# Kernel tuning notes

Hardware: AMD Instinct MI355X
Metric: run time of the kernel (lower is better)

## Reference

```python
import jax, jax.numpy as jnp
import numpy as np

HEADS = 2


def _log_cpb(h, w, w1, b1, w2):
    # Swin-v2 style continuous relative position bias on an h*w grid.
    yy, xx = jnp.meshgrid(jnp.arange(h), jnp.arange(w), indexing='ij')
    coords = jnp.stack([yy.reshape(-1), xx.reshape(-1)], axis=-1).astype(jnp.float32)  # (L, 2)
    rel = coords[:, None, :] - coords[None, :, :]                                      # (L, L, 2)
    denom = jnp.array([max(h - 1, 1), max(w - 1, 1)], dtype=jnp.float32)
    rel = rel / denom * 8.0
    rel = jnp.sign(rel) * jnp.log2(1.0 + jnp.abs(rel)) / np.float32(np.log2(8.0))
    bias = jax.nn.relu(rel @ w1.T + b1) @ w2.T                                         # (L, L, heads)
    return jnp.transpose(bias, (2, 0, 1))                                              # (heads, L, L)


def setup_inputs() -> dict:
    key = jax.random.key(0)
    ks = jax.random.split(key, 11)
    b, s, c, h, w = 2, 32, 128, 24, 24
    hid, out_ch = 256, 128
    sc = lambda n: 1.0 / np.sqrt(n)
    return {
        'x':      jax.random.normal(ks[0], (b, s, c, h, w), jnp.float32),
        'qk_w':   jax.random.normal(ks[1], (2 * c, c), jnp.float32) * sc(c),
        'v_w':    jax.random.normal(ks[2], (hid, c), jnp.float32) * sc(c),
        'cpb_w1': jax.random.normal(ks[3], (c, 2), jnp.float32) * sc(2),
        'cpb_b1': jax.random.normal(ks[4], (c,), jnp.float32) * 0.02,
        'cpb_w2': jax.random.normal(ks[5], (HEADS, c), jnp.float32) * sc(c),
        'sa_bias': jax.random.uniform(ks[6], (hid, 1, 1), jnp.float32, -sc(c), sc(c)),
        'mlp_w1': jax.random.normal(ks[7], (hid, hid), jnp.float32) * sc(hid),
        'mlp_b1': jax.random.normal(ks[8], (hid,), jnp.float32) * 0.02,
        'mlp_w2': jax.random.normal(ks[9], (out_ch, hid), jnp.float32) * sc(hid),
        'mlp_b2': jax.random.normal(ks[10], (out_ch,), jnp.float32) * 0.02,
    }


def reference(x, qk_w, v_w, cpb_w1, cpb_b1, cpb_w2, sa_bias, mlp_w1, mlp_b1, mlp_w2, mlp_b2):
    b, s, c, h, w = x.shape
    L = h * w
    qkd = c // HEADS
    vd = v_w.shape[0] // HEADS
    xr = x.reshape(b * s, c, L)                                        # flatten (b s) and (h w)
    # QKV via 1x1 convs == channel matmuls
    qk = jnp.einsum('oc,bcl->bol', qk_w, xr)                           # (bs, 2c, L)
    qk = qk.reshape(b * s, 2, HEADS, qkd, L).transpose(1, 0, 2, 4, 3)  # (2, bs, heads, L, d)
    q, k = qk[0], qk[1]
    v = jnp.einsum('oc,bcl->bol', v_w, xr).reshape(b * s, HEADS, vd, L).transpose(0, 1, 3, 2)
    # learned continuous relative position bias, added as SDPA attn_mask
    bias = _log_cpb(h, w, cpb_w1, cpb_b1, cpb_w2)                      # (heads, L, L)
    scale = np.float32(1.0 / np.sqrt(qkd))
    scores = jnp.einsum('bhld,bhmd->bhlm', q, k) * scale + bias[None]
    attn = jax.nn.softmax(scores, axis=-1)
    out = jnp.einsum('bhlm,bhmd->bhld', attn, v)                       # (bs, heads, L, vd)
    out = out.transpose(0, 1, 3, 2).reshape(b, s, HEADS * vd, h, w)
    out = out + sa_bias[None, None]                                    # (b, s, hid, h, w)
    # 1x1-conv MLP with exact GELU
    y = jnp.einsum('oi,bsihw->bsohw', mlp_w1, out) + mlp_b1[None, None, :, None, None]
    y = jax.nn.gelu(y, approximate=False)
    y = jnp.einsum('oi,bsihw->bsohw', mlp_w2, y) + mlp_b2[None, None, :, None, None]
    return y
```

## Files before the change

kernel.cpp:

```cpp
#include <hip/hip_runtime.h>
#include <cstdint>
#include <cstddef>

constexpr int BS   = 64;
constexpr int Cc   = 128;
constexpr int Lc   = 576;
constexpr int VD   = 128;
constexpr int HID  = 256;
constexpr int OUTC = 128;
constexpr int NPIX = BS * Lc;

typedef __bf16 bf16x8 __attribute__((ext_vector_type(8)));
typedef float  f32x4  __attribute__((ext_vector_type(4)));
typedef unsigned short u16x8 __attribute__((ext_vector_type(8)));
typedef unsigned int   u32x4 __attribute__((ext_vector_type(4)));

__device__ __forceinline__ unsigned short f2bf(float f) {
  unsigned int u = __builtin_bit_cast(unsigned int, f);
  u += 0x7fffu + ((u >> 16) & 1u);
  return (unsigned short)(u >> 16);
}
__device__ __forceinline__ float bf2f(unsigned short h) {
  unsigned int u = ((unsigned int)h) << 16;
  return __builtin_bit_cast(float, u);
}
__device__ __forceinline__ unsigned int packhl(float v) {
  unsigned short hi = f2bf(v);
  unsigned short lo = f2bf(v - bf2f(hi));
  return ((unsigned int)hi << 16) | (unsigned int)lo;
}
__device__ __forceinline__ void unpack8(u32x4 a, u32x4 b, bf16x8& hi, bf16x8& lo) {
  u32x4 h, l;
  h[0] = (a[1] & 0xffff0000u) | (a[0] >> 16);
  l[0] = (a[1] << 16)         | (a[0] & 0xffffu);
  h[1] = (a[3] & 0xffff0000u) | (a[2] >> 16);
  l[1] = (a[3] << 16)         | (a[2] & 0xffffu);
  h[2] = (b[1] & 0xffff0000u) | (b[0] >> 16);
  l[2] = (b[1] << 16)         | (b[0] & 0xffffu);
  h[3] = (b[3] & 0xffff0000u) | (b[2] >> 16);
  l[3] = (b[3] << 16)         | (b[2] & 0xffffu);
  hi = __builtin_bit_cast(bf16x8, h);
  lo = __builtin_bit_cast(bf16x8, l);
}

#define MFMA16(a, b, c) __builtin_amdgcn_mfma_f32_16x16x32_bf16((a), (b), (c), 0, 0, 0)

__global__ __launch_bounds__(256) void cpb_kernel(const float* __restrict__ w1,
                                                  const float* __restrict__ b1,
                                                  const float* __restrict__ w2,
                                                  float* __restrict__ tab) {
  int idx = blockIdx.x * 256 + threadIdx.x;
  if (idx >= 47 * 47) return;
  int dy = idx / 47 - 23, dx = idx % 47 - 23;
  float fy = (float)dy * (8.0f / 23.0f);
  float fx = (float)dx * (8.0f / 23.0f);
  fy = copysignf(log2f(1.0f + fabsf(fy)) * (1.0f / 3.0f), fy);
  fx = copysignf(log2f(1.0f + fabsf(fx)) * (1.0f / 3.0f), fx);
  float a0 = 0.f, a1 = 0.f;
  for (int hh = 0; hh < 128; hh++) {
    float hv = fmaxf(w1[2 * hh] * fy + w1[2 * hh + 1] * fx + b1[hh], 0.f);
    a0 += w2[hh] * hv;
    a1 += w2[128 + hh] * hv;
  }
  tab[idx] = a0;
  tab[2209 + idx] = a1;
}

__global__ __launch_bounds__(256) void bias_mat(const float* __restrict__ tab,
                                                unsigned short* __restrict__ biasC) {
  int id = blockIdx.x * 256 + threadIdx.x;
  if (id >= 737280) return;
  int id2 = id % 2560;
  int grp = id / 2560;
  int wave = grp & 3;
  int mt = (grp >> 2) % 36;
  int hh = grp / 144;
  int g = id2 / 512;
  int lane = (id2 >> 3) & 63;
  int k = id2 & 7;
  int e = g * 8 + k;
  unsigned short val = 0;
  if (e < 36) {
    int ln = e >> 2, r = e & 3;
    int nt = wave * 9 + ln;
    int i = mt * 16 + (lane >> 4) * 4 + r;
    int j = nt * 16 + (lane & 15);
    int yi = i / 24, xi = i - yi * 24;
    int yj = j / 24, xj = j - yj * 24;
    val = f2bf(tab[hh * 2209 + (yi - yj + 23) * 47 + (xi - xj + 23)]);
  }
  biasC[id] = val;
}

__global__ __launch_bounds__(256) void prep_w(
    const float* __restrict__ w1, const float* __restrict__ w2,
    const float* __restrict__ qkw, const float* __restrict__ vw,
    unsigned short* __restrict__ w1h, unsigned short* __restrict__ w1l,
    unsigned short* __restrict__ w2h, unsigned short* __restrict__ w2l,
    unsigned short* __restrict__ wqkh, unsigned short* __restrict__ wqkl,
    unsigned short* __restrict__ wvh, unsigned short* __restrict__ wvl) {
  int id = blockIdx.x * 256 + threadIdx.x;
  const float* src;
  unsigned short *dh, *dl;
  int off;
  if (id < 65536)       { src = w1;  dh = w1h;  dl = w1l;  off = id; }
  else if (id < 98304)  { src = w2;  dh = w2h;  dl = w2l;  off = id - 65536; }
  else if (id < 131072) { src = qkw; dh = wqkh; dl = wqkl; off = id - 98304; }
  else if (id < 163840) { src = vw;  dh = wvh;  dl = wvl;  off = id - 131072; }
  else return;
  float v = src[off];
  unsigned short hi = f2bf(v);
  dh[off] = hi;
  dl[off] = f2bf(v - bf2f(hi));
}

__global__ __launch_bounds__(256) void prep_x(const float* __restrict__ x,
                                              unsigned short* __restrict__ xph,
                                              unsigned short* __restrict__ xpl) {
  __shared__ float xt[128 * 65];
  const int l0 = blockIdx.x * 64, bs = blockIdx.y;
  const int t = threadIdx.x;
  const float* xb = x + (size_t)bs * Cc * Lc;
#pragma unroll
  for (int pass = 0; pass < 8; pass++) {
    int f = pass * 1024 + t * 4;
    int c = f >> 6, ll = f & 63;
    *(float4*)(xt + c * 65 + ll) = *(const float4*)(xb + c * Lc + l0 + ll);
  }
  __syncthreads();
  const int rowl = t >> 2, c0 = (t & 3) * 32;
  const size_t p = (size_t)bs * Lc + l0 + rowl;
  unsigned short hbuf[32], lbuf[32];
#pragma unroll
  for (int i = 0; i < 32; i++) {
    float v = xt[(c0 + i) * 65 + rowl];
    unsigned short hi = f2bf(v);
    hbuf[i] = hi;
    lbuf[i] = f2bf(v - bf2f(hi));
  }
#pragma unroll
  for (int g = 0; g < 4; g++) {
    *(u16x8*)(xph + p * 128 + c0 + g * 8) = *(u16x8*)(hbuf + g * 8);
    *(u16x8*)(xpl + p * 128 + c0 + g * 8) = *(u16x8*)(lbuf + g * 8);
  }
}

__global__ __launch_bounds__(256, 2) void qkv_mfma(
    const unsigned short* __restrict__ xh, const unsigned short* __restrict__ xl,
    const unsigned short* __restrict__ wqkh, const unsigned short* __restrict__ wqkl,
    const unsigned short* __restrict__ wvh, const unsigned short* __restrict__ wvl,
    unsigned short* __restrict__ qg, unsigned short* __restrict__ kg,
    unsigned short* __restrict__ vg) {
  __shared__ unsigned short vt[128 * 130];
  const int t = threadIdx.x;
  const int wv = t >> 6, lane = t & 63;
  const int quad = lane >> 4, cc = lane & 15;
  const int by = blockIdx.y;
  const int m0 = blockIdx.x * 128 + (wv & 1) * 64;
  const int n0 = (wv >> 1) * 64;
  const unsigned short* Wh = (by < 2) ? wqkh : wvh;
  const unsigned short* Wl = (by < 2) ? wqkl : wvl;
  const int wrow0 = (by & 1) * 128 + n0;
  f32x4 acc[4][4];
#pragma unroll
  for (int i = 0; i < 4; i++)
#pragma unroll
    for (int j = 0; j < 4; j++) acc[i][j] = (f32x4){0.f, 0.f, 0.f, 0.f};
  for (int kc = 0; kc < 4; kc++) {
    const int kb = kc * 32 + quad * 8;
    bf16x8 Ah[4], Al[4], Bh[4], Bl[4];
#pragma unroll
    for (int i = 0; i < 4; i++) {
      size_t ar = (size_t)(m0 + i * 16 + cc) * 128 + kb;
      Ah[i] = *(const bf16x8*)(xh + ar);
      Al[i] = *(const bf16x8*)(xl + ar);
      size_t br = (size_t)(wrow0 + i * 16 + cc) * 128 + kb;
      Bh[i] = *(const bf16x8*)(Wh + br);
      Bl[i] = *(const bf16x8*)(Wl + br);
    }
#pragma unroll
    for (int i = 0; i < 4; i++)
#pragma unroll
      for (int j = 0; j < 4; j++) {
        acc[i][j] = MFMA16(Ah[i], Bh[j], acc[i][j]);
        acc[i][j] = MFMA16(Al[i], Bh[j], acc[i][j]);
        acc[i][j] = MFMA16(Ah[i], Bl[j], acc[i][j]);
      }
  }
  if (by < 2) {
    const float sc = (by == 0) ? 0.125f : 1.0f;
#pragma unroll
    for (int j = 0; j < 4; j++) {
      int o = n0 + j * 16 + cc;
#pragma unroll
      for (int i = 0; i < 4; i++)
#pragma unroll
        for (int r = 0; r < 4; r++) {
          int pl = (wv & 1) * 64 + i * 16 + quad * 4 + r;
          vt[pl * 130 + o] = f2bf(acc[i][j][r] * sc);
        }
    }
    __syncthreads();
    unsigned short* dst = (by == 0) ? qg : kg;
    const int pl = t >> 1, head = t & 1;
    const int p = blockIdx.x * 128 + pl;
    const int bs = p / 576, l = p - bs * 576;
    unsigned short* drow = dst + ((size_t)(bs * 2 + head) * Lc + l) * 64;
#pragma unroll
    for (int g = 0; g < 8; g++)
      *(u16x8*)(drow + g * 8) = *(const u16x8*)(vt + pl * 130 + head * 64 + g * 8);
  } else {
    const int head = by - 2;
#pragma unroll
    for (int j = 0; j < 4; j++) {
      int d = n0 + j * 16 + cc;
#pragma unroll
      for (int i = 0; i < 4; i++)
#pragma unroll
        for (int r = 0; r < 4; r++) {
          int pl = (wv & 1) * 64 + i * 16 + quad * 4 + r;
          vt[d * 130 + pl] = f2bf(acc[i][j][r]);
        }
    }
    __syncthreads();
    const int d = t >> 1, half = (t & 1) * 64;
#pragma unroll
    for (int c8 = 0; c8 < 8; c8++) {
      int pl = half + c8 * 8;
      int p = blockIdx.x * 128 + pl;
      int bs = p / 576, l = p - bs * 576;
      *(u16x8*)(vg + ((size_t)(bs * 2 + head) * VD + d) * Lc + l) =
          *(u16x8*)(vt + d * 130 + pl);
    }
  }
}

__global__ __launch_bounds__(256, 4) void attn_kernel(
    const unsigned short* __restrict__ qg,
    const unsigned short* __restrict__ kg,
    const unsigned short* __restrict__ vg,
    const unsigned short* __restrict__ biasC,
    const float* __restrict__ sa_bias,
    unsigned int* __restrict__ aout_p) {
  constexpr int PP = 580;
  __shared__ unsigned short Pb[32 * PP];
  __shared__ float psum[4][32];
  const int pair = blockIdx.x;
  const int hh = pair & 1, bs = pair >> 1;
  const int bm = blockIdx.y;
  const int m0 = bm * 32;
  const int t = threadIdx.x;
  const int wv = t >> 6, lane = t & 63;
  const int quad = lane >> 4, c = lane & 15;
  const unsigned short* qb = qg + ((size_t)pair * Lc + m0) * 64;
  const unsigned short* kb = kg + (size_t)pair * Lc * 64;
  const unsigned short* vb = vg + (size_t)pair * VD * Lc;
  bf16x8 qa0[2], qa1[2];
#pragma unroll
  for (int mt = 0; mt < 2; mt++) {
    const unsigned short* qp = qb + (size_t)(mt * 16 + c) * 64 + quad * 8;
    qa0[mt] = *(const bf16x8*)qp;
    qa1[mt] = *(const bf16x8*)(qp + 32);
  }
  f32x4 S[2][9];
#pragma unroll
  for (int mt = 0; mt < 2; mt++) {
    const unsigned short* bbase =
        biasC + ((((size_t)hh * 36 + (bm * 2 + mt)) * 4 + wv) * 5) * 512;
#pragma unroll
    for (int g = 0; g < 5; g++) {
      u16x8 bv = *(const u16x8*)(bbase + g * 512 + lane * 8);
#pragma unroll
      for (int k = 0; k < 8; k++) {
        int e = g * 8 + k;
        if (e < 36) S[mt][e >> 2][e & 3] = bf2f(bv[k]);
      }
    }
  }
#pragma unroll
  for (int ln = 0; ln < 9; ln++) {
    int nt = wv * 9 + ln;
    const unsigned short* kp = kb + (size_t)(nt * 16 + c) * 64 + quad * 8;
    bf16x8 b0 = *(const bf16x8*)kp;
    bf16x8 b1 = *(const bf16x8*)(kp + 32);
#pragma unroll
    for (int mt = 0; mt < 2; mt++)
      S[mt][ln] = MFMA16(qa1[mt], b1, MFMA16(qa0[mt], b0, S[mt][ln]));
  }
  float sm[2][4] = {{0.f, 0.f, 0.f, 0.f}, {0.f, 0.f, 0.f, 0.f}};
#pragma unroll
  for (int mt = 0; mt < 2; mt++)
#pragma unroll
    for (int ln = 0; ln < 9; ln++)
#pragma unroll
      for (int r = 0; r < 4; r++) {
        float e = __expf(S[mt][ln][r]);
        sm[mt][r] += e;
        Pb[(mt * 16 + quad * 4 + r) * PP + (wv * 9 + ln) * 16 + c] = f2bf(e);
      }
#pragma unroll
  for (int sh = 1; sh < 16; sh <<= 1)
#pragma unroll
    for (int mt = 0; mt < 2; mt++)
#pragma unroll
      for (int r = 0; r < 4; r++) sm[mt][r] += __shfl_xor(sm[mt][r], sh);
  if (c == 0)
#pragma unroll
    for (int mt = 0; mt < 2; mt++)
#pragma unroll
      for (int r = 0; r < 4; r++)
        psum[wv][mt * 16 + quad * 4 + r] = sm[mt][r];
  __syncthreads();
  float inv[2][4];
#pragma unroll
  for (int mt = 0; mt < 2; mt++)
#pragma unroll
    for (int r = 0; r < 4; r++) {
      int row = mt * 16 + quad * 4 + r;
      inv[mt][r] =
          1.0f / (psum[0][row] + psum[1][row] + psum[2][row] + psum[3][row]);
    }
  const int nd0 = wv * 2;
  f32x4 O[2][2];
#pragma unroll
  for (int mt = 0; mt < 2; mt++)
#pragma unroll
    for (int dd = 0; dd < 2; dd++) O[mt][dd] = (f32x4){0.f, 0.f, 0.f, 0.f};
#pragma unroll
  for (int kc = 0; kc < 18; kc++) {
    bf16x8 pa[2];
#pragma unroll
    for (int mt = 0; mt < 2; mt++)
      pa[mt] = *(const bf16x8*)(Pb + (size_t)(mt * 16 + c) * PP + kc * 32 +
                                quad * 8);
#pragma unroll
    for (int dd = 0; dd < 2; dd++) {
      bf16x8 vf = *(const bf16x8*)(vb + (size_t)((nd0 + dd) * 16 + c) * Lc +
                                   kc * 32 + quad * 8);
#pragma unroll
      for (int mt = 0; mt < 2; mt++) O[mt][dd] = MFMA16(pa[mt], vf, O[mt][dd]);
    }
  }
  unsigned int* obp = aout_p + ((size_t)bs * Lc + m0) * HID + hh * 128;
#pragma unroll
  for (int dd = 0; dd < 2; dd++) {
    float sb = sa_bias[hh * 128 + (nd0 + dd) * 16 + c];
#pragma unroll
    for (int mt = 0; mt < 2; mt++)
#pragma unroll
      for (int r = 0; r < 4; r++) {
        float v = O[mt][dd][r] * inv[mt][r] + sb;
        obp[(size_t)(mt * 16 + quad * 4 + r) * HID + (nd0 + dd) * 16 + c] =
            packhl(v);
      }
  }
}

__global__ __launch_bounds__(256, 4) void mlp_fused(
    const unsigned int* __restrict__ ap,
    const unsigned short* __restrict__ w1h, const unsigned short* __restrict__ w1l,
    const float* __restrict__ b1,
    const unsigned short* __restrict__ w2h, const unsigned short* __restrict__ w2l,
    const float* __restrict__ b2, float* __restrict__ out) {
  constexpr int YPW = 260;
  __shared__ unsigned int lds[32 * YPW];
  const int t = threadIdx.x;
  const int wv = t >> 6, lane = t & 63;
  const int quad = lane >> 4, cc = lane & 15;
  const int c7 = cc & 7;
  const int M0 = blockIdx.x * 32;

  const unsigned int* gsrc = ap + (size_t)(M0 + 8 * wv + (lane >> 3)) * HID +
                             (((lane & 7) ^ (lane >> 3)) << 2);
  __builtin_amdgcn_global_load_lds(
      (const __attribute__((address_space(1))) unsigned int*)gsrc,
      (__attribute__((address_space(3))) unsigned int*)(&lds[wv * 256]),
      16, 0, 0);

  const int n0 = wv * 64;
  f32x4 acc1[2][4];
#pragma unroll
  for (int i = 0; i < 2; i++)
#pragma unroll
    for (int j = 0; j < 4; j++) acc1[i][j] = (f32x4){0.f, 0.f, 0.f, 0.f};
  for (int kc = 0; kc < 8; kc++) {
    __syncthreads();
    const int bufw = (kc & 1) << 10;
    bf16x8 Ah[2], Al[2];
#pragma unroll
    for (int i = 0; i < 2; i++) {
      const int row = i * 16 + cc;
      u32x4 pa = *(const u32x4*)&lds[bufw + row * 32 + (((2 * quad) ^ c7) << 2)];
      u32x4 pb =
          *(const u32x4*)&lds[bufw + row * 32 + (((2 * quad + 1) ^ c7) << 2)];
      unpack8(pa, pb, Ah[i], Al[i]);
    }
    if (kc < 7) {
      __builtin_amdgcn_global_load_lds(
          (const __attribute__((address_space(1))) unsigned int*)(gsrc +
                                                                  (kc + 1) * 32),
          (__attribute__((address_space(3))) unsigned int*)(
              &lds[(((kc + 1) & 1) << 10) + wv * 256]),
          16, 0, 0);
    }
    const int kb = kc * 32 + quad * 8;
    bf16x8 Bh[4], Bl[4];
#pragma unroll
    for (int j = 0; j < 4; j++) {
      size_t br = (size_t)(n0 + j * 16 + cc) * HID + kb;
      Bh[j] = *(const bf16x8*)(w1h + br);
      Bl[j] = *(const bf16x8*)(w1l + br);
    }
#pragma unroll
    for (int i = 0; i < 2; i++)
#pragma unroll
      for (int j = 0; j < 4; j++) {
        acc1[i][j] = MFMA16(Ah[i], Bh[j], acc1[i][j]);
        acc1[i][j] = MFMA16(Al[i], Bh[j], acc1[i][j]);
        acc1[i][j] = MFMA16(Ah[i], Bl[j], acc1[i][j]);
      }
  }
  __syncthreads();
#pragma unroll
  for (int j = 0; j < 4; j++) {
    int col = n0 + j * 16 + cc;
    float bias = b1[col];
#pragma unroll
    for (int i = 0; i < 2; i++)
#pragma unroll
      for (int r = 0; r < 4; r++) {
        int row = i * 16 + quad * 4 + r;
        float v = acc1[i][j][r] + bias;
        float g = 0.5f * v * (1.0f + erff(v * 0.70710678118654752f));
        lds[row * YPW + col] = packhl(g);
      }
  }
  __syncthreads();
  {
    const int n2 = wv * 32;
    f32x4 acc2[2][2];
#pragma unroll
    for (int i = 0; i < 2; i++)
#pragma unroll
      for (int j = 0; j < 2; j++) acc2[i][j] = (f32x4){0.f, 0.f, 0.f, 0.f};
    for (int kc = 0; kc < 8; kc++) {
      const int kb = kc * 32 + quad * 8;
      bf16x8 Ah[2], Al[2], Bh[2], Bl[2];
#pragma unroll
      for (int i = 0; i < 2; i++) {
        const unsigned int* arow = &lds[(i * 16 + cc) * YPW + kb];
        u32x4 pa = *(const u32x4*)arow;
        u32x4 pb = *(const u32x4*)(arow + 4);
        unpack8(pa, pb, Ah[i], Al[i]);
      }
#pragma unroll
      for (int j = 0; j < 2; j++) {
        size_t br = (size_t)(n2 + j * 16 + cc) * HID + kb;
        Bh[j] = *(const bf16x8*)(w2h + br);
        Bl[j] = *(const bf16x8*)(w2l + br);
      }
#pragma unroll
      for (int i = 0; i < 2; i++)
#pragma unroll
        for (int j = 0; j < 2; j++) {
          acc2[i][j] = MFMA16(Ah[i], Bh[j], acc2[i][j]);
          acc2[i][j] = MFMA16(Al[i], Bh[j], acc2[i][j]);
          acc2[i][j] = MFMA16(Ah[i], Bl[j], acc2[i][j]);
        }
    }
#pragma unroll
    for (int i = 0; i < 2; i++) {
      int p = M0 + i * 16 + quad * 4;
      int bs = p / Lc, l = p - bs * Lc;
#pragma unroll
      for (int j = 0; j < 2; j++) {
        int col = n2 + j * 16 + cc;
        float bias = b2[col];
        float4 v = make_float4(acc2[i][j][0] + bias, acc2[i][j][1] + bias,
                               acc2[i][j][2] + bias, acc2[i][j][3] + bias);
        *(float4*)(out + ((size_t)bs * OUTC + col) * Lc + l) = v;
      }
    }
  }
}

extern "C" void kernel_launch(void* const* d_in, const int* in_sizes, int n_in,
                              void* d_out, int out_size, void* d_ws, size_t ws_size,
                              hipStream_t stream) {
  const float* x    = (const float*)d_in[0];
  const float* qk_w = (const float*)d_in[1];
  const float* v_w  = (const float*)d_in[2];
  const float* cw1  = (const float*)d_in[3];
  const float* cb1  = (const float*)d_in[4];
  const float* cw2  = (const float*)d_in[5];
  const float* sab  = (const float*)d_in[6];
  const float* mw1  = (const float*)d_in[7];
  const float* mb1  = (const float*)d_in[8];
  const float* mw2  = (const float*)d_in[9];
  const float* mb2  = (const float*)d_in[10];
  float* out = (float*)d_out;
  char* ws = (char*)d_ws;

  float* tab = (float*)(ws);
  unsigned short* biasC  = (unsigned short*)(ws + 65536);
  unsigned short* qg     = (unsigned short*)(ws + 1572864);
  unsigned short* kg     = (unsigned short*)(ws + 11010048);
  unsigned short* vg     = (unsigned short*)(ws + 20447232);
  unsigned short* xph    = (unsigned short*)(ws + 39321600);
  unsigned short* xpl    = (unsigned short*)(ws + 48758784);
  unsigned int*   aout_p = (unsigned int*)(ws + 58195968);
  unsigned short* w1h    = (unsigned short*)(ws + 95944704);
  unsigned short* w1l    = (unsigned short*)(ws + 96075776);
  unsigned short* w2h    = (unsigned short*)(ws + 96206848);
  unsigned short* w2l    = (unsigned short*)(ws + 96272384);
  unsigned short* wqkh   = (unsigned short*)(ws + 96337920);
  unsigned short* wqkl   = (unsigned short*)(ws + 96403456);
  unsigned short* wvh    = (unsigned short*)(ws + 96468992);
  unsigned short* wvl    = (unsigned short*)(ws + 96534528);

  cpb_kernel<<<dim3(9), dim3(256), 0, stream>>>(cw1, cb1, cw2, tab);
  bias_mat<<<dim3(2880), dim3(256), 0, stream>>>(tab, biasC);
  prep_w<<<dim3(640), dim3(256), 0, stream>>>(mw1, mw2, qk_w, v_w,
                                              w1h, w1l, w2h, w2l,
                                              wqkh, wqkl, wvh, wvl);
  prep_x<<<dim3(9, 64), dim3(256), 0, stream>>>(x, xph, xpl);
  qkv_mfma<<<dim3(288, 4), dim3(256), 0, stream>>>(xph, xpl, wqkh, wqkl,
                                                   wvh, wvl, qg, kg, vg);
  attn_kernel<<<dim3(128, 18), dim3(256), 0, stream>>>(qg, kg, vg, biasC, sab,
                                                       aout_p);
  mlp_fused<<<dim3(1152), dim3(256), 0, stream>>>(aout_p, w1h, w1l, mb1,
                                                  w2h, w2l, mb2, out);
}
```

Before: 284.0 us.

## Stage QKV activation tiles through swizzled double-buffered LDS with async loads

The QKV projection kernel no longer has each wave read its x hi/lo A-fragments straight from global memory. The block now loads the 128-pixel tile into LDS once, using global_load_lds with an XOR swizzle, and double-buffers the next k-chunk while MFMAs run on the current one. This removes the duplicate global reads by the two waves that share rows and overlaps load latency with compute. It reuses the vt shared buffer, adds barriers, and depends on the barrier also waiting for the async LDS loads to finish.

Result: faster. 269.4 us (-5.1%).

```diff
diff --git a/kernel.cpp b/kernel.cpp
--- a/kernel.cpp
+++ b/kernel.cpp
@@ -156,7 +156,6 @@
   const int wv = t >> 6, lane = t & 63;
   const int quad = lane >> 4, cc = lane & 15;
   const int by = blockIdx.y;
-  const int m0 = blockIdx.x * 128 + (wv & 1) * 64;
   const int n0 = (wv >> 1) * 64;
   const unsigned short* Wh = (by < 2) ? wqkh : wvh;
   const unsigned short* Wl = (by < 2) ? wqkl : wvl;
@@ -166,27 +165,60 @@
   for (int i = 0; i < 4; i++)
 #pragma unroll
     for (int j = 0; j < 4; j++) acc[i][j] = (f32x4){0.f, 0.f, 0.f, 0.f};
-  for (int kc = 0; kc < 4; kc++) {
-    const int kb = kc * 32 + quad * 8;
-    bf16x8 Ah[4], Al[4], Bh[4], Bl[4];
-#pragma unroll
-    for (int i = 0; i < 4; i++) {
-      size_t ar = (size_t)(m0 + i * 16 + cc) * 128 + kb;
-      Ah[i] = *(const bf16x8*)(xh + ar);
-      Al[i] = *(const bf16x8*)(xl + ar);
-      size_t br = (size_t)(wrow0 + i * 16 + cc) * 128 + kb;
-      Bh[i] = *(const bf16x8*)(Wh + br);
-      Bl[i] = *(const bf16x8*)(Wl + br);
-    }
-#pragma unroll
-    for (int i = 0; i < 4; i++)
-#pragma unroll
-      for (int j = 0; j < 4; j++) {
-        acc[i][j] = MFMA16(Ah[i], Bh[j], acc[i][j]);
-        acc[i][j] = MFMA16(Al[i], Bh[j], acc[i][j]);
-        acc[i][j] = MFMA16(Ah[i], Bl[j], acc[i][j]);
-      }
-  }
+  {
+    const int srow = lane >> 3;
+    const int schunk = (lane & 7) ^ srow;
+    const size_t grow = (size_t)(blockIdx.x * 128 + wv * 32 + srow) * 128;
+    const unsigned short* asrc = (schunk < 4)
+                                     ? (xh + grow + (schunk << 3))
+                                     : (xl + grow + ((schunk - 4) << 3));
+    unsigned short* adst = vt + wv * 2048;
+#pragma unroll
+    for (int s = 0; s < 4; s++)
+      __builtin_amdgcn_global_load_lds(
+          (const __attribute__((address_space(1))) unsigned int*)(asrc + s * 1024),
+          (__attribute__((address_space(3))) unsigned int*)(adst + s * 512),
+          16, 0, 0);
+    for (int kc = 0; kc < 4; kc++) {
+      __syncthreads();
+      const int bufo = (kc & 1) << 13;
+      bf16x8 Ah[4], Al[4], Bh[4], Bl[4];
+#pragma unroll
+      for (int i = 0; i < 4; i++) {
+        const int row = (wv & 1) * 64 + i * 16 + cc;
+        const unsigned short* ab = vt + bufo + row * 64;
+        Ah[i] = *(const bf16x8*)(ab + ((quad ^ (cc & 7)) << 3));
+        Al[i] = *(const bf16x8*)(ab + (((quad + 4) ^ (cc & 7)) << 3));
+      }
+      if (kc < 3) {
+        const int nb = ((kc + 1) & 1) << 13;
+#pragma unroll
+        for (int s = 0; s < 4; s++)
+          __builtin_amdgcn_global_load_lds(
+              (const __attribute__((address_space(1))) unsigned int*)(
+                  asrc + (kc + 1) * 32 + s * 1024),
+              (__attribute__((address_space(3))) unsigned int*)(adst + nb +
+                                                                s * 512),
+              16, 0, 0);
+      }
+      const int kb = kc * 32 + quad * 8;
+#pragma unroll
+      for (int i = 0; i < 4; i++) {
+        size_t br = (size_t)(wrow0 + i * 16 + cc) * 128 + kb;
+        Bh[i] = *(const bf16x8*)(Wh + br);
+        Bl[i] = *(const bf16x8*)(Wl + br);
+      }
+#pragma unroll
+      for (int i = 0; i < 4; i++)
+#pragma unroll
+        for (int j = 0; j < 4; j++) {
+          acc[i][j] = MFMA16(Ah[i], Bh[j], acc[i][j]);
+          acc[i][j] = MFMA16(Al[i], Bh[j], acc[i][j]);
+          acc[i][j] = MFMA16(Ah[i], Bl[j], acc[i][j]);
+        }
+    }
+  }
+  __syncthreads();
   if (by < 2) {
     const float sc = (by == 0) ? 0.125f : 1.0f;
 #pragma unroll
```
